# Performance work log

Hardware: AMD Instinct MI355X
Metric: run time of the kernel (lower is better)

## Reference

```python
import jax, jax.numpy as jnp
import numpy as np

B, H, W, C = 128, 256, 1024, 1
N_HOLES = 5
PROB = 1.0
HOLE_MINW, HOLE_MAXW = W // 10, int(W / 2.5)   # 102, 409
HOLE_MINH, HOLE_MAXH = H // 10, int(H / 2.5)   # 25, 102


def setup_inputs() -> dict:
    key = jax.random.key(0)
    k0, k1, k2, k3, k4, k5 = jax.random.split(key, 6)
    x = jax.random.normal(k0, (B, H, W, C), dtype=jnp.float32)
    # hole centers: tf.random.uniform((bsz,n), 0, dim-1, int32) -> [0, dim-1)
    xs = jax.random.randint(k1, (B, N_HOLES), 0, W - 1, dtype=jnp.int32)
    ys = jax.random.randint(k2, (B, N_HOLES), 0, H - 1, dtype=jnp.int32)
    # hole sizes: raw in [0, max-min); reference adds the min offset
    xs_w_raw = jax.random.randint(k3, (B, N_HOLES), 0, HOLE_MAXW - HOLE_MINW, dtype=jnp.int32)
    ys_h_raw = jax.random.randint(k4, (B, N_HOLES), 0, HOLE_MAXH - HOLE_MINH, dtype=jnp.int32)
    # per-hole activation uniforms (hole active iff act_rand < PROB)
    act_rand = jax.random.uniform(k5, (B, N_HOLES), dtype=jnp.float32)
    return {"x": x, "xs": xs, "ys": ys, "xs_w_raw": xs_w_raw,
            "ys_h_raw": ys_h_raw, "act_rand": act_rand}


def _build_mask(xs, ys, xs_w_raw, ys_h_raw, act_rand):
    xs_w = xs_w_raw + HOLE_MINW                      # (B, N) hole widths
    ys_h = ys_h_raw + HOLE_MINH                      # (B, N) hole heights
    xs_start = jnp.clip(xs - xs_w // 2, 0, W - 2)
    xs_end   = jnp.clip(xs + xs_w // 2, 1, W - 1)
    ys_start = jnp.clip(ys - ys_h // 2, 0, H - 2)
    ys_end   = jnp.clip(ys + ys_h // 2, 1, H - 1)
    act = act_rand < PROB                            # (B, N) hole-wise activation
    idx_h = jnp.arange(H)
    idx_w = jnp.arange(W)
    mask = jnp.zeros((B, H, W), dtype=bool)
    for n in range(N_HOLES):                         # small fixed hole count
        mh = (ys_start[:, n, None] <= idx_h) & (idx_h <= ys_end[:, n, None])  # (B, H)
        mw = (xs_start[:, n, None] <= idx_w) & (idx_w <= xs_end[:, n, None])  # (B, W)
        m = mh[:, :, None] & mw[:, None, :]                                   # (B, H, W)
        mask = mask | (m & act[:, n, None, None])
    return mask


def reference(x, xs, ys, xs_w_raw, ys_h_raw, act_rand):
    mask = _build_mask(xs, ys, xs_w_raw, ys_h_raw, act_rand)   # (B, H, W) bool
    maskf = mask[..., None].astype(x.dtype)                    # (B, H, W, 1)
    fill = jnp.mean(x)  # hole_fill='min' path: hf = ones * reduce_mean(x)
    return x * (1.0 - maskf) + maskf * fill
```

## Files before the change

### kernel.cpp

```cpp
#include <hip/hip_runtime.h>


#define BB 128
#define HH 256
#define WW 1024
#define N_HOLES 5
#define HOLE_MINW (WW / 10)
#define HOLE_MINH (HH / 10)
#define N_ELEM (BB * HH * WW)
#define ROWS_PER_BLOCK 16
#define RED_BLOCKS (BB * HH / ROWS_PER_BLOCK)
#define ROW_SLICES 8

__global__ __launch_bounds__(256) void copy_reduce_kernel(
    const float* __restrict__ x, float* __restrict__ out,
    const int* __restrict__ xs, const int* __restrict__ ys,
    const int* __restrict__ xs_w_raw, const int* __restrict__ ys_h_raw,
    const float* __restrict__ act_rand,
    float* __restrict__ partials) {
  int blk = blockIdx.x;
  int b = blk >> 4;
  int row0 = blk * ROWS_PER_BLOCK;

  int ys_s[N_HOLES], ys_e[N_HOLES], xlo[N_HOLES], xhi[N_HOLES];
  #pragma unroll
  for (int n = 0; n < N_HOLES; ++n) {
    int base = b * N_HOLES + n;
    int cx = xs[base];
    int cy = ys[base];
    int hw = (xs_w_raw[base] + HOLE_MINW) >> 1;
    int hh = (ys_h_raw[base] + HOLE_MINH) >> 1;
    bool act = act_rand[base] < 1.0f;
    int yss = min(max(cy - hh, 0), HH - 2);
    int yse = min(max(cy + hh, 1), HH - 1);
    ys_s[n] = act ? yss : 1;
    ys_e[n] = act ? yse : 0;
    xlo[n] = min(max(cx - hw, 0), WW - 2);
    xhi[n] = min(max(cx + hw, 1), WW - 1);
  }

  const float4* x4 = (const float4*)x;
  float4* out4 = (float4*)out;
  int tid = threadIdx.x;
  int w0 = tid * 4;

  float s = 0.0f;
  for (int rr = 0; rr < ROWS_PER_BLOCK; ++rr) {
    int row = row0 + rr;
    int h = row & (HH - 1);
    long i = (long)row * (WW / 4) + tid;
    float4 v = x4[i];
    s += (v.x + v.y) + (v.z + v.w);

    bool all_hole = true;
    #pragma unroll
    for (int j = 0; j < 4; ++j) {
      int w = w0 + j;
      bool m = false;
      #pragma unroll
      for (int n = 0; n < N_HOLES; ++n) {
        bool in_row = (ys_s[n] <= h) && (h <= ys_e[n]);
        m = m || (in_row && (xlo[n] <= w) && (w <= xhi[n]));
      }
      all_hole = all_hole && m;
    }
    if (!all_hole) out4[i] = v;
  }

  #pragma unroll
  for (int off = 32; off > 0; off >>= 1) s += __shfl_down(s, off, 64);
  __shared__ float wsum[4];
  int lane = threadIdx.x & 63;
  int wave = threadIdx.x >> 6;
  if (lane == 0) wsum[wave] = s;
  __syncthreads();
  if (threadIdx.x == 0)
    partials[blockIdx.x] = (wsum[0] + wsum[1]) + (wsum[2] + wsum[3]);
}

__global__ __launch_bounds__(256) void fill_holes_kernel(
    const int* __restrict__ xs, const int* __restrict__ ys,
    const int* __restrict__ xs_w_raw, const int* __restrict__ ys_h_raw,
    const float* __restrict__ act_rand,
    const float* __restrict__ partials,
    float* __restrict__ out) {
  float s = 0.0f;
  for (int i = threadIdx.x; i < RED_BLOCKS; i += 256) s += partials[i];
  #pragma unroll
  for (int off = 32; off > 0; off >>= 1) s += __shfl_down(s, off, 64);
  __shared__ float wsum[4];
  __shared__ float mean_sh;
  int lane = threadIdx.x & 63;
  int wave = threadIdx.x >> 6;
  if (lane == 0) wsum[wave] = s;
  __syncthreads();
  if (threadIdx.x == 0) {
    float t = (wsum[0] + wsum[1]) + (wsum[2] + wsum[3]);
    mean_sh = t * (1.0f / (float)N_ELEM);
  }
  __syncthreads();
  float mean = mean_sh;

  int bid = blockIdx.x;
  int b = bid / (N_HOLES * ROW_SLICES);
  int rem = bid % (N_HOLES * ROW_SLICES);
  int n = rem / ROW_SLICES;
  int slice = rem % ROW_SLICES;

  int base = b * N_HOLES + n;
  if (!(act_rand[base] < 1.0f)) return;
  int cx = xs[base];
  int cy = ys[base];
  int hw = (xs_w_raw[base] + HOLE_MINW) >> 1;
  int hh = (ys_h_raw[base] + HOLE_MINH) >> 1;
  int ys_s = min(max(cy - hh, 0), HH - 2);
  int ys_e = min(max(cy + hh, 1), HH - 1);
  int xs_s = min(max(cx - hw, 0), WW - 2);
  int xs_e = min(max(cx + hw, 1), WW - 1);

  for (int h = ys_s + slice; h <= ys_e; h += ROW_SLICES) {
    long rowbase = (long)(b * HH + h) * WW;
    for (int w = xs_s + (int)threadIdx.x; w <= xs_e; w += 256) {
      out[rowbase + w] = mean;
    }
  }
}

extern "C" void kernel_launch(void* const* d_in, const int* in_sizes, int n_in,
                              void* d_out, int out_size, void* d_ws, size_t ws_size,
                              hipStream_t stream) {
  const float* x        = (const float*)d_in[0];
  const int* xs         = (const int*)d_in[1];
  const int* ys         = (const int*)d_in[2];
  const int* xs_w_raw   = (const int*)d_in[3];
  const int* ys_h_raw   = (const int*)d_in[4];
  const float* act_rand = (const float*)d_in[5];
  float* out = (float*)d_out;

  float* partials = (float*)d_ws;

  copy_reduce_kernel<<<RED_BLOCKS, 256, 0, stream>>>(
      x, out, xs, ys, xs_w_raw, ys_h_raw, act_rand, partials);
  fill_holes_kernel<<<BB * N_HOLES * ROW_SLICES, 256, 0, stream>>>(
      xs, ys, xs_w_raw, ys_h_raw, act_rand, partials, out);
}
```

Measured before the change: 266.8 us.

## Fuse copy-reduce and hole fill into one cooperative kernel with grid sync

Merges the copy/partial-sum pass and the hole-fill pass into a single cooperative kernel of 1024 persistent blocks. Each block handles 32 rows, writes two partial sums, waits at a grid-wide barrier, recomputes the mean and then fills its share of hole rectangles. This removes the second kernel launch and the gap between kernels, at the cost of a grid-sync barrier and less parallelism per block in the streaming phase. If the cooperative launch fails, it falls back to the original two-kernel path.

```diff
diff --git a/kernel.cpp b/kernel.cpp
--- a/kernel.cpp
+++ b/kernel.cpp
@@ -1,4 +1,7 @@
 #include <hip/hip_runtime.h>
+#include <hip/hip_cooperative_groups.h>
+
+namespace cg = cooperative_groups;
 
 
 #define BB 128
@@ -11,16 +14,24 @@
 #define ROWS_PER_BLOCK 16
 #define RED_BLOCKS (BB * HH / ROWS_PER_BLOCK)
 #define ROW_SLICES 8
-
-__global__ __launch_bounds__(256) void copy_reduce_kernel(
+#define FBLOCKS 1024
+#define FROWS 32
+#define FILL_UNITS (BB * N_HOLES * ROW_SLICES)
+
+__global__ __launch_bounds__(256, 4) void fused_kernel(
     const float* __restrict__ x, float* __restrict__ out,
     const int* __restrict__ xs, const int* __restrict__ ys,
     const int* __restrict__ xs_w_raw, const int* __restrict__ ys_h_raw,
     const float* __restrict__ act_rand,
     float* __restrict__ partials) {
   int blk = blockIdx.x;
-  int b = blk >> 4;
-  int row0 = blk * ROWS_PER_BLOCK;
+  int b = blk >> 3;
+  int row0 = blk * FROWS;
+  int tid = threadIdx.x;
+  int lane = tid & 63;
+  int wave = tid >> 6;
+  __shared__ float wsum[4];
+  __shared__ float mean_sh;
 
   int ys_s[N_HOLES], ys_e[N_HOLES], xlo[N_HOLES], xhi[N_HOLES];
   #pragma unroll
@@ -41,6 +52,113 @@
 
   const float4* x4 = (const float4*)x;
   float4* out4 = (float4*)out;
+  int w0 = tid * 4;
+
+  #pragma unroll
+  for (int g = 0; g < 2; ++g) {
+    float s = 0.0f;
+    for (int rr = 0; rr < ROWS_PER_BLOCK; ++rr) {
+      int row = row0 + g * ROWS_PER_BLOCK + rr;
+      int h = row & (HH - 1);
+      long i = (long)row * (WW / 4) + tid;
+      float4 v = x4[i];
+      s += (v.x + v.y) + (v.z + v.w);
+
+      bool all_hole = true;
+      #pragma unroll
+      for (int j = 0; j < 4; ++j) {
+        int w = w0 + j;
+        bool m = false;
+        #pragma unroll
+        for (int n = 0; n < N_HOLES; ++n) {
+          bool in_row = (ys_s[n] <= h) && (h <= ys_e[n]);
+          m = m || (in_row && (xlo[n] <= w) && (w <= xhi[n]));
+        }
+        all_hole = all_hole && m;
+      }
+      if (!all_hole) out4[i] = v;
+    }
+    #pragma unroll
+    for (int off = 32; off > 0; off >>= 1) s += __shfl_down(s, off, 64);
+    if (lane == 0) wsum[wave] = s;
+    __syncthreads();
+    if (tid == 0)
+      partials[2 * blk + g] = (wsum[0] + wsum[1]) + (wsum[2] + wsum[3]);
+    __syncthreads();
+  }
+
+  cg::this_grid().sync();
+
+  {
+    float s = 0.0f;
+    for (int i = tid; i < RED_BLOCKS; i += 256) s += partials[i];
+    #pragma unroll
+    for (int off = 32; off > 0; off >>= 1) s += __shfl_down(s, off, 64);
+    if (lane == 0) wsum[wave] = s;
+    __syncthreads();
+    if (tid == 0) {
+      float t = (wsum[0] + wsum[1]) + (wsum[2] + wsum[3]);
+      mean_sh = t * (1.0f / (float)N_ELEM);
+    }
+    __syncthreads();
+  }
+  float mean = mean_sh;
+
+  for (int u = blk; u < FILL_UNITS; u += FBLOCKS) {
+    int b2 = u / (N_HOLES * ROW_SLICES);
+    int rem = u % (N_HOLES * ROW_SLICES);
+    int n = rem / ROW_SLICES;
+    int slice = rem % ROW_SLICES;
+
+    int base = b2 * N_HOLES + n;
+    if (!(act_rand[base] < 1.0f)) continue;
+    int cx = xs[base];
+    int cy = ys[base];
+    int hw = (xs_w_raw[base] + HOLE_MINW) >> 1;
+    int hh = (ys_h_raw[base] + HOLE_MINH) >> 1;
+    int yss = min(max(cy - hh, 0), HH - 2);
+    int yse = min(max(cy + hh, 1), HH - 1);
+    int xss = min(max(cx - hw, 0), WW - 2);
+    int xse = min(max(cx + hw, 1), WW - 1);
+
+    for (int h = yss + slice; h <= yse; h += ROW_SLICES) {
+      long rowbase = (long)(b2 * HH + h) * WW;
+      for (int w = xss + tid; w <= xse; w += 256) {
+        out[rowbase + w] = mean;
+      }
+    }
+  }
+}
+
+__global__ __launch_bounds__(256) void copy_reduce_kernel(
+    const float* __restrict__ x, float* __restrict__ out,
+    const int* __restrict__ xs, const int* __restrict__ ys,
+    const int* __restrict__ xs_w_raw, const int* __restrict__ ys_h_raw,
+    const float* __restrict__ act_rand,
+    float* __restrict__ partials) {
+  int blk = blockIdx.x;
+  int b = blk >> 4;
+  int row0 = blk * ROWS_PER_BLOCK;
+
+  int ys_s[N_HOLES], ys_e[N_HOLES], xlo[N_HOLES], xhi[N_HOLES];
+  #pragma unroll
+  for (int n = 0; n < N_HOLES; ++n) {
+    int base = b * N_HOLES + n;
+    int cx = xs[base];
+    int cy = ys[base];
+    int hw = (xs_w_raw[base] + HOLE_MINW) >> 1;
+    int hh = (ys_h_raw[base] + HOLE_MINH) >> 1;
+    bool act = act_rand[base] < 1.0f;
+    int yss = min(max(cy - hh, 0), HH - 2);
+    int yse = min(max(cy + hh, 1), HH - 1);
+    ys_s[n] = act ? yss : 1;
+    ys_e[n] = act ? yse : 0;
+    xlo[n] = min(max(cx - hw, 0), WW - 2);
+    xhi[n] = min(max(cx + hw, 1), WW - 1);
+  }
+
+  const float4* x4 = (const float4*)x;
+  float4* out4 = (float4*)out;
   int tid = threadIdx.x;
   int w0 = tid * 4;
 
@@ -139,8 +257,15 @@
 
   float* partials = (float*)d_ws;
 
-  copy_reduce_kernel<<<RED_BLOCKS, 256, 0, stream>>>(
-      x, out, xs, ys, xs_w_raw, ys_h_raw, act_rand, partials);
-  fill_holes_kernel<<<BB * N_HOLES * ROW_SLICES, 256, 0, stream>>>(
-      xs, ys, xs_w_raw, ys_h_raw, act_rand, partials, out);
-}
+  void* args[] = {(void*)&x, (void*)&out, (void*)&xs, (void*)&ys,
+                  (void*)&xs_w_raw, (void*)&ys_h_raw, (void*)&act_rand,
+                  (void*)&partials};
+  hipError_t err = hipLaunchCooperativeKernel(
+      (const void*)fused_kernel, dim3(FBLOCKS), dim3(256), args, 0, stream);
+  if (err != hipSuccess) {
+    copy_reduce_kernel<<<RED_BLOCKS, 256, 0, stream>>>(
+        x, out, xs, ys, xs_w_raw, ys_h_raw, act_rand, partials);
+    fill_holes_kernel<<<BB * N_HOLES * ROW_SLICES, 256, 0, stream>>>(
+        xs, ys, xs_w_raw, ys_h_raw, act_rand, partials, out);
+  }
+}
```

Measured after the change: 390.2 us. 1.46x slower.
